# Optimization experiments

Hardware: AMD Instinct MI355X
Metric: run time of the kernel (lower is better)

## Reference

```python
import jax, jax.numpy as jnp
import numpy as np
from jax import lax

B = 2; C = 256; NH = 8; NP = 4; NUM_LAYERS = 6; FFN = 1024
IN_SIZES = (512, 1024, 2048)
LVL_SHAPES = ((64, 64), (32, 32), (16, 16), (8, 8), (4, 4))
NL = len(LVL_SHAPES); DH = C // NH
N = sum(h * w for h, w in LVL_SHAPES)  # 5456 tokens over the pyramid


def _ln(x, g, b):
    m = x.mean(-1, keepdims=True)
    v = x.var(-1, keepdims=True)
    return (x - m) * lax.rsqrt(v + 1e-5) * g + b


def _gn(x, g, b, groups=8):
    Bb, Cc, Hh, Ww = x.shape
    xr = x.reshape(Bb, groups, Cc // groups, Hh, Ww)
    m = xr.mean((2, 3, 4), keepdims=True)
    v = xr.var((2, 3, 4), keepdims=True)
    xr = (xr - m) * lax.rsqrt(v + 1e-5)
    return xr.reshape(Bb, Cc, Hh, Ww) * g[None, :, None, None] + b[None, :, None, None]


def _conv(x, w, b, stride, pad):
    y = lax.conv_general_dilated(x, w, (stride, stride), [(pad, pad), (pad, pad)],
                                 dimension_numbers=('NCHW', 'OIHW', 'NCHW'))
    return y + b[None, :, None, None]


def _priors():
    # normalized (cx, cy) anchor centers per pyramid location
    pr = []
    for (fh, fw) in LVL_SHAPES:
        cy = (jnp.arange(fh, dtype=jnp.float32) + 0.5) / fh
        cx = (jnp.arange(fw, dtype=jnp.float32) + 0.5) / fw
        gy, gx = jnp.meshgrid(cy, cx, indexing='ij')
        pr.append(jnp.stack([gx, gy], -1).reshape(-1, 2))
    return jnp.concatenate(pr, 0)  # [N,2]


def _sample(vl, loc, fh, fw):
    # vl: [B,NH,S_l,DH] flattened level values; loc: [B,N,NH,NP,2] in [0,1]
    x = loc[..., 0] * fw - 0.5
    y = loc[..., 1] * fh - 0.5
    x0 = jnp.floor(x); y0 = jnp.floor(y)
    lx = x - x0; ly = y - y0

    def gather(xi, yi):
        inb = ((xi >= 0) & (xi <= fw - 1) & (yi >= 0) & (yi <= fh - 1)).astype(vl.dtype)
        xc = jnp.clip(xi, 0, fw - 1).astype(jnp.int32)
        yc = jnp.clip(yi, 0, fh - 1).astype(jnp.int32)
        idx = (yc * fw + xc).transpose(0, 2, 1, 3).reshape(B, NH, N * NP)
        g = jnp.take_along_axis(vl, idx[..., None], axis=2)  # [B,NH,N*NP,DH]
        g = g.reshape(B, NH, N, NP, DH).transpose(0, 2, 1, 3, 4)  # [B,N,NH,NP,DH]
        return g * inb[..., None]

    return (gather(x0, y0) * ((1 - lx) * (1 - ly))[..., None]
            + gather(x0 + 1, y0) * (lx * (1 - ly))[..., None]
            + gather(x0, y0 + 1) * ((1 - lx) * ly)[..., None]
            + gather(x0 + 1, y0 + 1) * (lx * ly)[..., None])


def _attn_layer(x, priors, g1, b1_, woff, boff, watt, batt, wval, bval, wout, bout):
    q = _ln(x, g1, b1_)
    off = (q @ woff + boff).reshape(B, N, NH, NL, NP, 2)
    att = jax.nn.softmax((q @ watt + batt).reshape(B, N, NH, NL * NP), axis=-1)
    att = att.reshape(B, N, NH, NL, NP)
    val = (q @ wval + bval).reshape(B, N, NH, DH)
    normz = jnp.array([[w, h] for (h, w) in LVL_SHAPES], jnp.float32)  # (W,H) per level
    loc = priors[None, :, None, None, None, :] + off / normz[None, None, None, :, None, :]
    out = jnp.zeros((B, N, NH, DH), x.dtype)
    start = 0
    for l, (fh, fw) in enumerate(LVL_SHAPES):
        vl = val[:, start:start + fh * fw].transpose(0, 2, 1, 3)  # [B,NH,S_l,DH]
        s = _sample(vl, loc[:, :, :, l], fh, fw)  # [B,N,NH,NP,DH]
        out = out + (s * att[:, :, :, l, :, None]).sum(3)
        start += fh * fw
    return x + out.reshape(B, N, C) @ wout + bout


def _ffn(x, g2, b2_, w1, b1_, w2, b2_2):
    h = jax.nn.relu(_ln(x, g2, b2_) @ w1 + b1_)
    return x + h @ w2 + b2_2


def _forward(in_map0, in_map1, in_map2, pw0, pb0, pw1, pb1, pw2, pb2,
             buw0, bub0, gng, gnb, buw1, bub1,
             ln1g, ln1b, woff, boff, watt, batt, wval, bval, wout, bout,
             ln2g, ln2b, w1, b1, w2, b2):
    maps = [_conv(in_map0, pw0, pb0, 1, 0), _conv(in_map1, pw1, pb1, 1, 0), _conv(in_map2, pw2, pb2, 1, 0)]
    m = _conv(in_map2, buw0, bub0, 2, 1)  # bottom-up from raw C5 (2048ch)
    maps.append(m)
    m = _conv(jax.nn.relu(_gn(m, gng, gnb)), buw1, bub1, 2, 1)
    maps.append(m)
    feats = jnp.concatenate([mm.reshape(B, C, -1).transpose(0, 2, 1) for mm in maps], axis=1)  # [B,N,C]
    priors = _priors()
    for i in range(NUM_LAYERS):
        feats = _attn_layer(feats, priors, ln1g[i], ln1b[i], woff[i], boff[i],
                            watt[i], batt[i], wval[i], bval[i], wout[i], bout[i])
        feats = _ffn(feats, ln2g[i], ln2b[i], w1[i], b1[i], w2[i], b2[i])
    return feats


def setup_inputs():
    key = jax.random.key(0)
    ks = list(jax.random.split(key, 40)); ki = iter(ks)
    def rn(shape, s=0.02):
        return jax.random.normal(next(ki), shape, jnp.float32) * s
    inp = {}
    for i, (cs, (h, w)) in enumerate(zip(IN_SIZES, LVL_SHAPES[:3])):
        inp[f"in_map{i}"] = jax.random.normal(next(ki), (B, cs, h, w), jnp.float32)
    for i, cs in enumerate(IN_SIZES):
        inp[f"pw{i}"] = rn((C, cs, 1, 1)); inp[f"pb{i}"] = jnp.zeros((C,), jnp.float32)
    inp["buw0"] = rn((C, IN_SIZES[-1], 3, 3)); inp["bub0"] = jnp.zeros((C,), jnp.float32)
    inp["gng"] = jnp.ones((C,), jnp.float32); inp["gnb"] = jnp.zeros((C,), jnp.float32)
    inp["buw1"] = rn((C, C, 3, 3)); inp["bub1"] = jnp.zeros((C,), jnp.float32)
    LYR = NUM_LAYERS
    inp["ln1g"] = jnp.ones((LYR, C), jnp.float32); inp["ln1b"] = jnp.zeros((LYR, C), jnp.float32)
    inp["woff"] = rn((LYR, C, NH * NL * NP * 2), 0.01)
    th = np.arange(NH) * (2.0 * np.pi / NH)
    grid = np.stack([np.cos(th), np.sin(th)], -1)
    grid = grid / np.abs(grid).max(-1, keepdims=True)  # [NH,2]
    boff = np.tile(grid[:, None, None, :], (1, NL, NP, 1)) * (np.arange(NP) + 1)[None, None, :, None]
    inp["boff"] = jnp.tile(jnp.asarray(boff.reshape(-1), jnp.float32)[None], (LYR, 1))
    inp["watt"] = rn((LYR, C, NH * NL * NP), 0.01); inp["batt"] = jnp.zeros((LYR, NH * NL * NP), jnp.float32)
    inp["wval"] = rn((LYR, C, C)); inp["bval"] = jnp.zeros((LYR, C), jnp.float32)
    inp["wout"] = rn((LYR, C, C)); inp["bout"] = jnp.zeros((LYR, C), jnp.float32)
    inp["ln2g"] = jnp.ones((LYR, C), jnp.float32); inp["ln2b"] = jnp.zeros((LYR, C), jnp.float32)
    inp["w1"] = rn((LYR, C, FFN)); inp["b1"] = jnp.zeros((LYR, FFN), jnp.float32)
    inp["w2"] = rn((LYR, FFN, C)); inp["b2"] = jnp.zeros((LYR, C), jnp.float32)
    return inp


def reference(in_map0, in_map1, in_map2, pw0, pb0, pw1, pb1, pw2, pb2,
              buw0, bub0, gng, gnb, buw1, bub1,
              ln1g, ln1b, woff, boff, watt, batt, wval, bval, wout, bout,
              ln2g, ln2b, w1, b1, w2, b2):
    feats = _forward(in_map0, in_map1, in_map2, pw0, pb0, pw1, pb1, pw2, pb2,
                     buw0, bub0, gng, gnb, buw1, bub1,
                     ln1g, ln1b, woff, boff, watt, batt, wval, bval, wout, bout,
                     ln2g, ln2b, w1, b1, w2, b2)
    outs = []
    start = 0
    for (fh, fw) in LVL_SHAPES:
        outs.append(feats[:, start:start + fh * fw].transpose(0, 2, 1).reshape(B, C, fh, fw))
        start += fh * fw
    return tuple(outs)
```

## Files before the change

### kernel.cpp

```cpp
#include <hip/hip_runtime.h>
#include <cstdint>

typedef long long i64;
typedef unsigned short u16;
typedef __attribute__((ext_vector_type(8))) short short8;
typedef __attribute__((ext_vector_type(8))) unsigned short us8;
typedef __attribute__((ext_vector_type(4))) float f32x4;

#define NTOK 5456
#define BNROWS 10912
#define NLAYERS 6

__device__ __forceinline__ u16 f2bf(float f) {
  unsigned u = __float_as_uint(f);
  return (u16)((u + 0x7FFFu + ((u >> 16) & 1u)) >> 16);
}
__device__ __forceinline__ float bf2f(u16 h) {
  return __uint_as_float(((unsigned)h) << 16);
}

template<int BNT>
__global__ __launch_bounds__(256) void mgemm_k(
    const u16* __restrict__ A, const u16* __restrict__ B, int K,
    float* __restrict__ C, float* __restrict__ C2, u16* __restrict__ C16, i64 sCm,
    const float* __restrict__ bias, int relu, int addres, int qkv,
    int M, int N, int mbsh, i64 bCz,
    int KS, float* __restrict__ part)
{
  constexpr int NW = BNT / 32;
  __shared__ u16 Asm[2][128 * 64];
  __shared__ u16 Bsm[2][BNT * 64];
  int tid = threadIdx.x;

  int bx = blockIdx.x, by = blockIdx.y;
  int gx = gridDim.x, gy = gridDim.y;
  int nwg = gx * gy;
  if (KS == 1 && nwg >= 16) {
    int lin = bx + gx * by;
    int xcd = lin & 7, k = lin >> 3;
    int q = nwg >> 3, r = nwg & 7;
    int f = (xcd < r) ? (xcd * (q + 1) + k) : (r * (q + 1) + (xcd - r) * q + k);
    bx = f / gy;
    by = f - bx * gy;
  }
  int m0 = bx * 128, n0 = by * BNT;

  int ks = blockIdx.z;
  int Kc = K / KS;
  int k0 = ks * Kc;
  int lane = tid & 63, w = tid >> 6;
  int wr = w >> 1, wc = w & 1;
  int r16 = lane & 15, g = lane >> 4;

  f32x4 acc[4][NW];
#pragma unroll
  for (int mi = 0; mi < 4; mi++)
#pragma unroll
    for (int nj = 0; nj < NW; nj++) acc[mi][nj] = (f32x4){0.f, 0.f, 0.f, 0.f};

  const u16* Ag = A + (i64)m0 * K + k0;
  const u16* Bg = B + (i64)n0 * K + k0;
  int nt = Kc >> 6;

  auto stage = [&](int buf, int kt) {
#pragma unroll
    for (int r = 0; r < 4; r++) {
      int s = r * 256 + tid;
      int row = s >> 3, c = s & 7;
      int cs = ((c ^ (row & 7)) << 3);
      __builtin_amdgcn_global_load_lds(
          (const __attribute__((address_space(1))) void*)(Ag + (i64)row * K + kt + cs),
          (__attribute__((address_space(3))) void*)(&Asm[buf][(r * 256 + (w << 6)) << 3]),
          16, 0, 0);
    }
#pragma unroll
    for (int r = 0; r < NW; r++) {
      int s = r * 256 + tid;
      int row = s >> 3, c = s & 7;
      int cs = ((c ^ (row & 7)) << 3);
      __builtin_amdgcn_global_load_lds(
          (const __attribute__((address_space(1))) void*)(Bg + (i64)row * K + kt + cs),
          (__attribute__((address_space(3))) void*)(&Bsm[buf][(r * 256 + (w << 6)) << 3]),
          16, 0, 0);
    }
  };

  stage(0, 0);
  __syncthreads();
  for (int t = 0; t < nt; t++) {
    int cur = t & 1;
    if (t + 1 < nt) stage(cur ^ 1, (t + 1) << 6);
#pragma unroll
    for (int h = 0; h < 2; h++) {
      short8 av[4], bv[NW];
#pragma unroll
      for (int mi = 0; mi < 4; mi++) {
        int row = wr * 64 + mi * 16 + r16;
        av[mi] = *(const short8*)&Asm[cur][row * 64 + ((((h << 2) + g) ^ (row & 7)) << 3)];
      }
#pragma unroll
      for (int nj = 0; nj < NW; nj++) {
        int row = wc * (NW * 16) + nj * 16 + r16;
        bv[nj] = *(const short8*)&Bsm[cur][row * 64 + ((((h << 2) + g) ^ (row & 7)) << 3)];
      }
#pragma unroll
      for (int mi = 0; mi < 4; mi++)
#pragma unroll
        for (int nj = 0; nj < NW; nj++)
          acc[mi][nj] = __builtin_amdgcn_mfma_f32_16x16x32_bf16(
              av[mi], bv[nj], acc[mi][nj], 0, 0, 0);
    }
    __syncthreads();
  }

  if (KS > 1) {
#pragma unroll
    for (int mi = 0; mi < 4; mi++)
#pragma unroll
      for (int nj = 0; nj < NW; nj++)
#pragma unroll
        for (int r = 0; r < 4; r++) {
          int grow = m0 + wr * 64 + mi * 16 + g * 4 + r;
          int gcol = n0 + wc * (NW * 16) + nj * 16 + r16;
          if (grow < M) part[((i64)ks * M + grow) * N + gcol] = acc[mi][nj][r];
        }
  } else if (qkv) {
    u16* off16 = (u16*)C;
    u16* att16 = (u16*)C2;
#pragma unroll
    for (int mi = 0; mi < 4; mi++)
#pragma unroll
      for (int nj = 0; nj < NW; nj++)
#pragma unroll
        for (int r = 0; r < 4; r++) {
          int grow = m0 + wr * 64 + mi * 16 + g * 4 + r;
          int gcol = n0 + wc * (NW * 16) + nj * 16 + r16;
          if (grow < M) {
            float v = acc[mi][nj][r] + bias[gcol];
            if (gcol < 320) off16[(i64)grow * 320 + gcol] = f2bf(v);
            else if (gcol < 480) att16[(i64)grow * 160 + (gcol - 320)] = f2bf(v);
            else if (gcol < 736) C16[(i64)grow * 256 + (gcol - 480)] = f2bf(v);
          }
        }
  } else {
    float bv[NW];
    int gc0 = n0 + wc * (NW * 16) + r16;
#pragma unroll
    for (int nj = 0; nj < NW; nj++)
      bv[nj] = bias ? bias[gc0 + nj * 16] : 0.f;
    int mask = (1 << mbsh) - 1;
#pragma unroll
    for (int mi = 0; mi < 4; mi++) {
#pragma unroll
      for (int r = 0; r < 4; r++) {
        int grow = m0 + wr * 64 + mi * 16 + g * 4 + r;
        if (grow >= M) continue;
        i64 rowb = (i64)(grow >> mbsh) * bCz + (i64)(grow & mask) * sCm;
#pragma unroll
        for (int nj = 0; nj < NW; nj++) {
          int gcol = gc0 + nj * 16;
          if (gcol >= N) continue;
          float v = acc[mi][nj][r] + bv[nj];
          if (relu) v = fmaxf(v, 0.f);
          i64 ci = rowb + gcol;
          if (C16) C16[ci] = f2bf(v);
          else {
            if (addres) v += C[ci];
            C[ci] = v;
          }
        }
      }
    }
  }
}

__global__ __launch_bounds__(256) void ffn_fused_k(
    const u16* __restrict__ qb, const u16* __restrict__ w1n,
    const u16* __restrict__ w2n, const float* __restrict__ b1,
    const float* __restrict__ b2, float* __restrict__ feats, int M)
{
  __shared__ u16 As[64 * 256];
  __shared__ u16 B1s[64 * 256];
  __shared__ u16 B2s[256 * 64];
  __shared__ u16 Hs[64 * 64];
  __shared__ float b1s[1024];
  int tid = threadIdx.x;
  int lane = tid & 63, w = tid >> 6;
  int wr = w >> 1, wc = w & 1;
  int r16 = lane & 15, g = lane >> 4;
  int m0 = blockIdx.x * 64;

  for (int i = tid; i < 1024; i += 256) b1s[i] = b1[i];

#pragma unroll
  for (int r = 0; r < 8; r++) {
    int s = r * 256 + tid;
    int row = s >> 5, c = s & 31;
    int cs = ((c ^ (row & 7)) << 3);
    __builtin_amdgcn_global_load_lds(
        (const __attribute__((address_space(1))) void*)(qb + (i64)(m0 + row) * 256 + cs),
        (__attribute__((address_space(3))) void*)(&As[(r * 256 + (w << 6)) << 3]),
        16, 0, 0);
  }

  f32x4 acc2[2][8];
#pragma unroll
  for (int mi = 0; mi < 2; mi++)
#pragma unroll
    for (int nj = 0; nj < 8; nj++) acc2[mi][nj] = (f32x4){0.f, 0.f, 0.f, 0.f};

  for (int ch = 0; ch < 16; ch++) {
#pragma unroll
    for (int r = 0; r < 8; r++) {
      int s = r * 256 + tid;
      int row = s >> 5, c = s & 31;
      int cs = ((c ^ (row & 7)) << 3);
      __builtin_amdgcn_global_load_lds(
          (const __attribute__((address_space(1))) void*)(w1n + (i64)(ch * 64 + row) * 256 + cs),
          (__attribute__((address_space(3))) void*)(&B1s[(r * 256 + (w << 6)) << 3]),
          16, 0, 0);
    }
#pragma unroll
    for (int r = 0; r < 8; r++) {
      int s = r * 256 + tid;
      int row = s >> 3, c = s & 7;
      int cs = ((c ^ (row & 7)) << 3);
      __builtin_amdgcn_global_load_lds(
          (const __attribute__((address_space(1))) void*)(w2n + (i64)row * 1024 + ch * 64 + cs),
          (__attribute__((address_space(3))) void*)(&B2s[(r * 256 + (w << 6)) << 3]),
          16, 0, 0);
    }
    __syncthreads();

    f32x4 acc1[2][2];
#pragma unroll
    for (int mi = 0; mi < 2; mi++)
#pragma unroll
      for (int nj = 0; nj < 2; nj++) acc1[mi][nj] = (f32x4){0.f, 0.f, 0.f, 0.f};
#pragma unroll
    for (int ks = 0; ks < 8; ks++) {
      short8 av[2], bv[2];
#pragma unroll
      for (int mi = 0; mi < 2; mi++) {
        int row = wr * 32 + mi * 16 + r16;
        av[mi] = *(const short8*)&As[row * 256 + ((((ks << 2) + g) ^ (row & 7)) << 3)];
      }
#pragma unroll
      for (int nj = 0; nj < 2; nj++) {
        int row = wc * 32 + nj * 16 + r16;
        bv[nj] = *(const short8*)&B1s[row * 256 + ((((ks << 2) + g) ^ (row & 7)) << 3)];
      }
#pragma unroll
      for (int mi = 0; mi < 2; mi++)
#pragma unroll
        for (int nj = 0; nj < 2; nj++)
          acc1[mi][nj] = __builtin_amdgcn_mfma_f32_16x16x32_bf16(
              av[mi], bv[nj], acc1[mi][nj], 0, 0, 0);
    }
#pragma unroll
    for (int mi = 0; mi < 2; mi++)
#pragma unroll
      for (int nj = 0; nj < 2; nj++)
#pragma unroll
        for (int r = 0; r < 4; r++) {
          int row_h = wr * 32 + mi * 16 + g * 4 + r;
          int col_h = wc * 32 + nj * 16 + r16;
          float v = acc1[mi][nj][r] + b1s[ch * 64 + col_h];
          v = fmaxf(v, 0.f);
          Hs[row_h * 64 + (((col_h >> 3) ^ (row_h & 7)) << 3) + (col_h & 7)] = f2bf(v);
        }
    __syncthreads();

#pragma unroll
    for (int hh = 0; hh < 2; hh++) {
      short8 av2[2], bv2[8];
#pragma unroll
      for (int mi = 0; mi < 2; mi++) {
        int row = wr * 32 + mi * 16 + r16;
        av2[mi] = *(const short8*)&Hs[row * 64 + ((((hh << 2) + g) ^ (row & 7)) << 3)];
      }
#pragma unroll
      for (int nj = 0; nj < 8; nj++) {
        int n = wc * 128 + nj * 16 + r16;
        bv2[nj] = *(const short8*)&B2s[n * 64 + ((((hh << 2) + g) ^ (n & 7)) << 3)];
      }
#pragma unroll
      for (int mi = 0; mi < 2; mi++)
#pragma unroll
        for (int nj = 0; nj < 8; nj++)
          acc2[mi][nj] = __builtin_amdgcn_mfma_f32_16x16x32_bf16(
              av2[mi], bv2[nj], acc2[mi][nj], 0, 0, 0);
    }
    __syncthreads();
  }

#pragma unroll
  for (int mi = 0; mi < 2; mi++)
#pragma unroll
    for (int r = 0; r < 4; r++) {
      int grow = m0 + wr * 32 + mi * 16 + g * 4 + r;
      if (grow >= M) continue;
#pragma unroll
      for (int nj = 0; nj < 8; nj++) {
        int col = wc * 128 + nj * 16 + r16;
        i64 ci = (i64)grow * 256 + col;
        feats[ci] += acc2[mi][nj][r] + b2[col];
      }
    }
}

__global__ void reduce_k(const float* __restrict__ part, float* __restrict__ C,
    const float* __restrict__ bias, int mbsh, i64 bCz, i64 sCm, int M, int N, int KS)
{
  int idx = blockIdx.x * 256 + threadIdx.x;
  if (idx >= M * N) return;
  int m = idx / N, n = idx - m * N;
  float v = bias ? bias[n] : 0.f;
  for (int ks = 0; ks < KS; ks++) v += part[((i64)ks * M + m) * N + n];
  C[(i64)(m >> mbsh) * bCz + (i64)(m & ((1 << mbsh) - 1)) * sCm + n] = v;
}

__global__ void cvt_w_pro_k(const float* __restrict__ pw0, const float* __restrict__ pw1,
    const float* __restrict__ pw2, const float* __restrict__ buw0,
    const float* __restrict__ buw1, u16* __restrict__ dst)
{
  int idx = blockIdx.x * 256 + threadIdx.x;
  if (idx >= 6225920) return;
  float v;
  if (idx < 131072) v = pw0[idx];
  else if (idx < 393216) v = pw1[idx - 131072];
  else if (idx < 917504) v = pw2[idx - 393216];
  else if (idx < 5636096) v = buw0[idx - 917504];
  else v = buw1[idx - 5636096];
  dst[idx] = f2bf(v);
}

__global__ void cvt_w_layer_k(const float* __restrict__ woff, const float* __restrict__ watt,
    const float* __restrict__ wval, const float* __restrict__ wout,
    const float* __restrict__ w1, const float* __restrict__ w2, u16* __restrict__ dst)
{
  int L = blockIdx.y;
  int o = blockIdx.x * 256 + threadIdx.x;
  if (o >= 786432) return;
  u16* d = dst + (i64)L * 786432;
  float v;
  if (o < 196608) {
    int n = o >> 8, k = o & 255;
    if (n < 320) v = woff[(i64)L * 81920 + k * 320 + n];
    else if (n < 480) v = watt[(i64)L * 40960 + k * 160 + (n - 320)];
    else if (n < 736) v = wval[(i64)L * 65536 + k * 256 + (n - 480)];
    else v = 0.f;
  } else if (o < 262144) {
    int o2 = o - 196608; int n = o2 >> 8, k = o2 & 255;
    v = wout[(i64)L * 65536 + k * 256 + n];
  } else if (o < 524288) {
    int o2 = o - 262144; int n = o2 >> 8, k = o2 & 255;
    v = w1[(i64)L * 262144 + (i64)k * 1024 + n];
  } else {
    int o2 = o - 524288; int n = o2 >> 10, k = o2 & 1023;
    v = w2[(i64)L * 262144 + (i64)k * 256 + n];
  }
  d[o] = f2bf(v);
}

__global__ void cvt_bias_k(const float* __restrict__ boff, const float* __restrict__ batt,
    const float* __restrict__ bval, float* __restrict__ bq)
{
  int idx = blockIdx.x * 256 + threadIdx.x;
  if (idx >= NLAYERS * 768) return;
  int L = idx / 768, n = idx - L * 768;
  float v;
  if (n < 320) v = boff[(i64)L * 320 + n];
  else if (n < 480) v = batt[(i64)L * 160 + (n - 320)];
  else if (n < 736) v = bval[(i64)L * 256 + (n - 480)];
  else v = 0.f;
  bq[idx] = v;
}

__global__ void cvt_a_proj_k(const float* __restrict__ in, u16* __restrict__ out,
                             int P, int K)
{
  i64 o = (i64)blockIdx.x * 256 + threadIdx.x;
  if (o >= (i64)2 * P * K) return;
  int m = (int)(o / K), k = (int)(o % K);
  int b = m / P, p = m - b * P;
  out[o] = f2bf(in[((i64)b * K + k) * P + p]);
}

__global__ void im2col_bf16_k(const float* __restrict__ in, u16* __restrict__ out,
    int Cin, int Hin, int Win, int Ho, int Wo)
{
  int Kk = Cin * 9;
  i64 total = (i64)2 * Ho * Wo * Kk;
  i64 o = (i64)blockIdx.x * 256 + threadIdx.x;
  if (o >= total) return;
  int k = (int)(o % Kk);
  int m = (int)(o / Kk);
  int hw = Ho * Wo;
  int b = m / hw, pix = m - b * hw;
  int oy = pix / Wo, ox = pix - oy * Wo;
  int ci = k / 9, r = k - ci * 9;
  int ky = r / 3, kx = r - ky * 3;
  int iy = oy * 2 - 1 + ky, ix = ox * 2 - 1 + kx;
  float v = 0.f;
  if (iy >= 0 && iy < Hin && ix >= 0 && ix < Win)
    v = in[(((i64)b * Cin + ci) * Hin + iy) * Win + ix];
  out[o] = f2bf(v);
}

__global__ void gn_relu_k(const float* __restrict__ feats, float* __restrict__ y,
    const float* __restrict__ g, const float* __restrict__ bt)
{
  int grp = blockIdx.x, b = blockIdx.y;
  int tid = threadIdx.x;
  const float* fb = feats + ((i64)b * NTOK + 5376) * 256 + grp * 32;
  float s = 0.f, ss = 0.f;
  for (int i = tid; i < 2048; i += 256) {
    int cl = i >> 6, p = i & 63;
    float v = fb[(i64)p * 256 + cl];
    s += v; ss += v * v;
  }
  __shared__ float sb[4], ssb[4];
#pragma unroll
  for (int o = 32; o > 0; o >>= 1) { s += __shfl_down(s, o); ss += __shfl_down(ss, o); }
  int wv = tid >> 6;
  if ((tid & 63) == 0) { sb[wv] = s; ssb[wv] = ss; }
  __syncthreads();
  float ts = sb[0] + sb[1] + sb[2] + sb[3];
  float tss = ssb[0] + ssb[1] + ssb[2] + ssb[3];
  float mean = ts * (1.f / 2048.f);
  float rs = rsqrtf(tss * (1.f / 2048.f) - mean * mean + 1e-5f);
  for (int i = tid; i < 2048; i += 256) {
    int cl = i >> 6, p = i & 63;
    int c = grp * 32 + cl;
    float v = (fb[(i64)p * 256 + cl] - mean) * rs * g[c] + bt[c];
    y[((i64)b * 256 + c) * 64 + p] = fmaxf(v, 0.f);
  }
}

__global__ __launch_bounds__(256) void ln_k(const float* __restrict__ x,
    u16* __restrict__ y, const float* __restrict__ g, const float* __restrict__ bt,
    int rows)
{
  int row = blockIdx.x * 4 + (threadIdx.x >> 6);
  if (row >= rows) return;
  int lane = threadIdx.x & 63;
  float4 v = ((const float4*)(x + (i64)row * 256))[lane];
  float s = v.x + v.y + v.z + v.w;
  float ss = v.x * v.x + v.y * v.y + v.z * v.z + v.w * v.w;
#pragma unroll
  for (int o = 32; o > 0; o >>= 1) { s += __shfl_down(s, o); ss += __shfl_down(ss, o); }
  s = __shfl(s, 0);
  ss = __shfl(ss, 0);
  float mean = s * (1.f / 256.f);
  float rs = rsqrtf(ss * (1.f / 256.f) - mean * mean + 1e-5f);
  float4 gg = ((const float4*)g)[lane];
  float4 bb = ((const float4*)bt)[lane];
  ushort4 o4;
  o4.x = f2bf((v.x - mean) * rs * gg.x + bb.x);
  o4.y = f2bf((v.y - mean) * rs * gg.y + bb.y);
  o4.z = f2bf((v.z - mean) * rs * gg.z + bb.z);
  o4.w = f2bf((v.w - mean) * rs * gg.w + bb.w);
  ((ushort4*)(y + (i64)row * 256))[lane] = o4;
}

__global__ __launch_bounds__(256) void dsample_k(
    const u16* __restrict__ val, const u16* __restrict__ off,
    const u16* __restrict__ att, u16* __restrict__ out)
{
  const int FH[5] = {64, 32, 16, 8, 4};
  const int ST[5] = {0, 4096, 5120, 5376, 5440};
  int bid = blockIdx.x;
  int chunk = (bid & 7) * 86 + (bid >> 3);
  if (chunk >= 682) return;
  int lane = threadIdx.x & 63;
  int half = lane >> 5;
  int l32 = lane & 31;
  int t = chunk * 8 + ((threadIdx.x >> 6) << 1) + half;
  int b = blockIdx.y;
  int h = l32 >> 2, d4 = l32 & 3;

  int lv;
  if (t < 4096)      lv = 0;
  else if (t < 5120) lv = 1;
  else if (t < 5376) lv = 2;
  else if (t < 5440) lv = 3;
  else               lv = 4;
  int loc = t - ST[lv];
  int sh = 6 - lv;
  int py = loc >> sh, px = loc - (py << sh);
  float inv = 1.f / (float)FH[lv];
  float prx = (px + 0.5f) * inv, pry = (py + 0.5f) * inv;
  i64 bt = (i64)b * NTOK + t;
  const u16* offp = off + bt * 320 + h * 40;
  const u16* attp = att + bt * 160 + h * 20;
  const u16* vbase = val + ((i64)b * NTOK) * 256 + h * 32 + d4 * 8;

  float own_a[5], own_fx[5], own_fy[5];
  int own_pk[5];
  float mx = -1e30f;
#pragma unroll
  for (int j = 0; j < 5; j++) {
    float lg = bf2f(attp[d4 + 4 * j]);
    own_a[j] = lg;
    mx = fmaxf(mx, lg);
  }
  mx = fmaxf(mx, __shfl_xor(mx, 1));
  mx = fmaxf(mx, __shfl_xor(mx, 2));
  float sum = 0.f;
#pragma unroll
  for (int j = 0; j < 5; j++) {
    float e = __expf(own_a[j] - mx);
    own_a[j] = e;
    sum += e;
  }
  sum += __shfl_xor(sum, 1);
  sum += __shfl_xor(sum, 2);
  float rinv = 1.f / sum;
#pragma unroll
  for (int j = 0; j < 5; j++) {
    int p = d4 + 4 * j;
    own_a[j] *= rinv;
    unsigned opk = *(const unsigned*)(offp + 2 * p);
    float ox = bf2f((u16)(opk & 0xFFFF));
    float oy = bf2f((u16)(opk >> 16));
    float sff = (float)(64 >> j);
    float xx = prx * sff + ox - 0.5f;
    float yy = pry * sff + oy - 0.5f;
    float xf = floorf(xx), yf = floorf(yy);
    own_fx[j] = xx - xf;
    own_fy[j] = yy - yf;
    own_pk[j] = (((int)yf) << 16) | (((int)xf) & 0xFFFF);
  }

  float acc[8] = {0.f, 0.f, 0.f, 0.f, 0.f, 0.f, 0.f, 0.f};
#pragma unroll
  for (int p = 0; p < 20; p++) {
    const int j = p >> 2;
    const int sf = FH[j], st = ST[j];
    int src = (half << 5) | (h << 2) | (p & 3);
    float wa = __shfl(own_a[j], src);
    float fx = __shfl(own_fx[j], src);
    float fy = __shfl(own_fy[j], src);
    int pk = __shfl(own_pk[j], src);
    int x0 = (pk << 16) >> 16;
    int y0 = pk >> 16;
    float gx0 = wa - wa * fx, gx1 = wa * fx;
    float w00 = gx0 - gx0 * fy, w01 = gx0 * fy;
    float w10 = gx1 - gx1 * fy, w11 = gx1 * fy;
    bool xin0 = (x0 >= 0) & (x0 < sf), xin1 = (x0 + 1 >= 0) & (x0 + 1 < sf);
    bool yin0 = (y0 >= 0) & (y0 < sf), yin1 = (y0 + 1 >= 0) & (y0 + 1 < sf);
    int ibase = st + y0 * sf + x0;
#define FMA8(W, IDX) { \
      us8 v = *(const us8*)(vbase + (i64)(IDX) * 256); \
      acc[0] = fmaf(W, bf2f(v[0]), acc[0]); acc[1] = fmaf(W, bf2f(v[1]), acc[1]); \
      acc[2] = fmaf(W, bf2f(v[2]), acc[2]); acc[3] = fmaf(W, bf2f(v[3]), acc[3]); \
      acc[4] = fmaf(W, bf2f(v[4]), acc[4]); acc[5] = fmaf(W, bf2f(v[5]), acc[5]); \
      acc[6] = fmaf(W, bf2f(v[6]), acc[6]); acc[7] = fmaf(W, bf2f(v[7]), acc[7]); }
    if (xin0 & yin0) FMA8(w00, ibase);
    if (xin1 & yin0) FMA8(w10, ibase + 1);
    if (xin0 & yin1) FMA8(w01, ibase + sf);
    if (xin1 & yin1) FMA8(w11, ibase + sf + 1);
#undef FMA8
  }
  us8 o;
#pragma unroll
  for (int i = 0; i < 8; i++) o[i] = f2bf(acc[i]);
  *(us8*)(out + ((bt * 8 + h) * 32 + d4 * 8)) = o;
}

__global__ __launch_bounds__(256) void untranspose_all_k(
    const float* __restrict__ feats, float* __restrict__ out)
{
  int u = blockIdx.x;
  int pt0, start, S; i64 ooff;
  if (u < 128)      { pt0 = u;       start = 0;    S = 4096; ooff = 0; }
  else if (u < 160) { pt0 = u - 128; start = 4096; S = 1024; ooff = 2097152; }
  else if (u < 168) { pt0 = u - 160; start = 5120; S = 256;  ooff = 2621440; }
  else if (u < 170) { pt0 = u - 168; start = 5376; S = 64;   ooff = 2752512; }
  else              { pt0 = 0;       start = 5440; S = 16;   ooff = 2785280; }
  __shared__ float tile[32][33];
  int pt = pt0 * 32, ct = blockIdx.y * 32, b = blockIdx.z;
  int tx = threadIdx.x & 31, ty = threadIdx.x >> 5;
  for (int i = ty; i < 32; i += 8) {
    int p = pt + i;
    tile[i][tx] = (p < S) ? feats[((i64)b * NTOK + start + p) * 256 + ct + tx] : 0.f;
  }
  __syncthreads();
  for (int i = ty; i < 32; i += 8) {
    int c = ct + i, p = pt + tx;
    if (p < S) out[ooff + ((i64)b * 256 + c) * S + p] = tile[tx][i];
  }
}

extern "C" void kernel_launch(void* const* d_in, const int* in_sizes, int n_in,
                              void* d_out, int out_size, void* d_ws, size_t ws_size,
                              hipStream_t stream)
{
  const float* in0  = (const float*)d_in[0];
  const float* in1  = (const float*)d_in[1];
  const float* in2  = (const float*)d_in[2];
  const float* pw0  = (const float*)d_in[3];
  const float* pb0  = (const float*)d_in[4];
  const float* pw1  = (const float*)d_in[5];
  const float* pb1  = (const float*)d_in[6];
  const float* pw2  = (const float*)d_in[7];
  const float* pb2  = (const float*)d_in[8];
  const float* buw0 = (const float*)d_in[9];
  const float* bub0 = (const float*)d_in[10];
  const float* gng  = (const float*)d_in[11];
  const float* gnb  = (const float*)d_in[12];
  const float* buw1 = (const float*)d_in[13];
  const float* bub1 = (const float*)d_in[14];
  const float* ln1g = (const float*)d_in[15];
  const float* ln1b = (const float*)d_in[16];
  const float* woff = (const float*)d_in[17];
  const float* boff = (const float*)d_in[18];
  const float* watt = (const float*)d_in[19];
  const float* batt = (const float*)d_in[20];
  const float* wval = (const float*)d_in[21];
  const float* bval = (const float*)d_in[22];
  const float* wout = (const float*)d_in[23];
  const float* bout = (const float*)d_in[24];
  const float* ln2g = (const float*)d_in[25];
  const float* ln2b = (const float*)d_in[26];
  const float* w1   = (const float*)d_in[27];
  const float* b1   = (const float*)d_in[28];
  const float* w2   = (const float*)d_in[29];
  const float* b2   = (const float*)d_in[30];
  float* out = (float*)d_out;

  const i64 TC = (i64)NTOK * 256;

  float* ws    = (float*)d_ws;
  float* feats = ws;
  u16*   qb    = (u16*)(feats + 2793472);
  u16*   valb  = qb + 2818048;
  u16*   sampb = valb + 2818048;
  float* U     = (float*)(sampb + 2818048);
  u16*   off16 = (u16*)U;
  u16*   att16 = off16 + 3491840;
  u16*   abuf  = (u16*)U;
  float* part  = U + 2097152;
  u16*   wb    = (u16*)(U + 5637120);
  float* bqkv  = (float*)(wb + 10944512);
  float* m4gn  = bqkv + 4608;

  auto mg128 = [&](dim3 grid, const u16* A, const u16* B, int K,
                   float* C, float* C2, u16* C16, i64 sCm, const float* bias,
                   int relu, int addres, int qkv, int M, int N, int mbsh, i64 bCz, int KS) {
    mgemm_k<128><<<grid, dim3(256), 0, stream>>>(A, B, K, C, C2, C16, sCm, bias,
        relu, addres, qkv, M, N, mbsh, bCz, KS, part);
  };
  auto mg64 = [&](dim3 grid, const u16* A, const u16* B, int K,
                  float* C, u16* C16, i64 sCm, const float* bias,
                  int relu, int addres, int M, int N, int mbsh, i64 bCz, int KS) {
    mgemm_k<64><<<grid, dim3(256), 0, stream>>>(A, B, K, C, nullptr, C16, sCm, bias,
        relu, addres, 0, M, N, mbsh, bCz, KS, part);
  };

  cvt_w_pro_k<<<dim3(24320), dim3(256), 0, stream>>>(pw0, pw1, pw2, buw0, buw1, wb);
  cvt_w_layer_k<<<dim3(3072, NLAYERS), dim3(256), 0, stream>>>(
      woff, watt, wval, wout, w1, w2, wb + 6225920);
  cvt_bias_k<<<dim3(18), dim3(256), 0, stream>>>(boff, batt, bval, bqkv);

  cvt_a_proj_k<<<dim3(16384), dim3(256), 0, stream>>>(in0, abuf, 4096, 512);
  mg64(dim3(64, 4, 1), abuf, wb, 512, feats, nullptr, 256, pb0, 0, 0,
       8192, 256, 12, TC, 1);
  cvt_a_proj_k<<<dim3(8192), dim3(256), 0, stream>>>(in1, abuf, 1024, 1024);
  mg64(dim3(16, 4, 2), abuf, wb + 131072, 1024, nullptr, nullptr, 256, nullptr, 0, 0,
       2048, 256, 10, 0, 2);
  reduce_k<<<dim3(2048), dim3(256), 0, stream>>>(part, feats + (i64)4096 * 256, pb1,
      10, TC, 256, 2048, 256, 2);
  cvt_a_proj_k<<<dim3(4096), dim3(256), 0, stream>>>(in2, abuf, 256, 2048);
  mg64(dim3(4, 4, 4), abuf, wb + 393216, 2048, nullptr, nullptr, 256, nullptr, 0, 0,
       512, 256, 8, 0, 4);
  reduce_k<<<dim3(512), dim3(256), 0, stream>>>(part, feats + (i64)5120 * 256, pb2,
      8, TC, 256, 512, 256, 4);

  im2col_bf16_k<<<dim3(9216), dim3(256), 0, stream>>>(in2, abuf, 2048, 16, 16, 8, 8);
  mg64(dim3(1, 4, 16), abuf, wb + 917504, 18432, nullptr, nullptr, 256, nullptr, 0, 0,
       128, 256, 6, 0, 16);
  reduce_k<<<dim3(128), dim3(256), 0, stream>>>(part, feats + (i64)5376 * 256, bub0,
      6, TC, 256, 128, 256, 16);

  gn_relu_k<<<dim3(8, 2), dim3(256), 0, stream>>>(feats, m4gn, gng, gnb);
  im2col_bf16_k<<<dim3(288), dim3(256), 0, stream>>>(m4gn, abuf, 256, 8, 8, 4, 4);
  mg64(dim3(1, 4, 4), abuf, wb + 5636096, 2304, nullptr, nullptr, 256, nullptr, 0, 0,
       32, 256, 4, 0, 4);
  reduce_k<<<dim3(32), dim3(256), 0, stream>>>(part, feats + (i64)5440 * 256, bub1,
      4, TC, 256, 32, 256, 4);

  for (int i = 0; i < NLAYERS; i++) {
    const u16* wbL = wb + 6225920 + (i64)i * 786432;
    ln_k<<<dim3(2728), dim3(256), 0, stream>>>(feats, qb,
        ln1g + (i64)i * 256, ln1b + (i64)i * 256, BNROWS);
    mg128(dim3(86, 6, 1), qb, wbL, 256, (float*)off16, (float*)att16, valb, 0,
          bqkv + (i64)i * 768, 0, 0, 1, BNROWS, 768, 14, 0, 1);
    dsample_k<<<dim3(688, 2), dim3(256), 0, stream>>>(valb, off16, att16, sampb);
    mg64(dim3(86, 4, 1), sampb, wbL + 196608, 256, feats, nullptr, 256,
         bout + (i64)i * 256, 0, 1, BNROWS, 256, 14, 0, 1);
    ln_k<<<dim3(2728), dim3(256), 0, stream>>>(feats, qb,
        ln2g + (i64)i * 256, ln2b + (i64)i * 256, BNROWS);
    ffn_fused_k<<<dim3(171), dim3(256), 0, stream>>>(qb, wbL + 262144,
        wbL + 524288, b1 + (i64)i * 1024, b2 + (i64)i * 256, feats, BNROWS);
  }

  untranspose_all_k<<<dim3(171, 8, 2), dim3(256), 0, stream>>>(feats, out);
  (void)in_sizes; (void)n_in; (void)out_size; (void)ws_size;
}
```

Measured before the change: 1.013 ms.

## Double-buffer FFN weight tiles and keep activation tile in registers

The fused FFN kernel now stages W1/W2 chunks into two LDS buffers, prefetching the next chunk while the current one is computed. This hides global-load latency behind the MFMA work. The input activation tile is loaded once directly into registers instead of LDS. The hidden tile uses a padded row stride instead of XOR swizzling. The trade-off is more LDS (about 147KB, which forces one block per CU via launch bounds) and more registers.

```diff
diff --git a/kernel.cpp b/kernel.cpp
--- a/kernel.cpp
+++ b/kernel.cpp
@@ -174,15 +174,14 @@
   }
 }
 
-__global__ __launch_bounds__(256) void ffn_fused_k(
+__global__ __launch_bounds__(256, 1) void ffn_fused_k(
     const u16* __restrict__ qb, const u16* __restrict__ w1n,
     const u16* __restrict__ w2n, const float* __restrict__ b1,
     const float* __restrict__ b2, float* __restrict__ feats, int M)
 {
-  __shared__ u16 As[64 * 256];
-  __shared__ u16 B1s[64 * 256];
-  __shared__ u16 B2s[256 * 64];
-  __shared__ u16 Hs[64 * 64];
+  __shared__ u16 B1s[2][64 * 256];
+  __shared__ u16 B2s[2][256 * 64];
+  __shared__ u16 Hs[64 * 88];
   __shared__ float b1s[1024];
   int tid = threadIdx.x;
   int lane = tid & 63, w = tid >> 6;
@@ -192,24 +191,16 @@
 
   for (int i = tid; i < 1024; i += 256) b1s[i] = b1[i];
 
-#pragma unroll
-  for (int r = 0; r < 8; r++) {
-    int s = r * 256 + tid;
-    int row = s >> 5, c = s & 31;
-    int cs = ((c ^ (row & 7)) << 3);
-    __builtin_amdgcn_global_load_lds(
-        (const __attribute__((address_space(1))) void*)(qb + (i64)(m0 + row) * 256 + cs),
-        (__attribute__((address_space(3))) void*)(&As[(r * 256 + (w << 6)) << 3]),
-        16, 0, 0);
-  }
-
-  f32x4 acc2[2][8];
-#pragma unroll
-  for (int mi = 0; mi < 2; mi++)
-#pragma unroll
-    for (int nj = 0; nj < 8; nj++) acc2[mi][nj] = (f32x4){0.f, 0.f, 0.f, 0.f};
-
-  for (int ch = 0; ch < 16; ch++) {
+  short8 av_all[8][2];
+#pragma unroll
+  for (int ks = 0; ks < 8; ks++)
+#pragma unroll
+    for (int mi = 0; mi < 2; mi++) {
+      int row = m0 + wr * 32 + mi * 16 + r16;
+      av_all[ks][mi] = *(const short8*)(qb + (i64)row * 256 + ks * 32 + g * 8);
+    }
+
+  auto stageW = [&](int buf, int ch) {
 #pragma unroll
     for (int r = 0; r < 8; r++) {
       int s = r * 256 + tid;
@@ -217,7 +208,7 @@
       int cs = ((c ^ (row & 7)) << 3);
       __builtin_amdgcn_global_load_lds(
           (const __attribute__((address_space(1))) void*)(w1n + (i64)(ch * 64 + row) * 256 + cs),
-          (__attribute__((address_space(3))) void*)(&B1s[(r * 256 + (w << 6)) << 3]),
+          (__attribute__((address_space(3))) void*)(&B1s[buf][(r * 256 + (w << 6)) << 3]),
           16, 0, 0);
     }
 #pragma unroll
@@ -227,10 +218,23 @@
       int cs = ((c ^ (row & 7)) << 3);
       __builtin_amdgcn_global_load_lds(
           (const __attribute__((address_space(1))) void*)(w2n + (i64)row * 1024 + ch * 64 + cs),
-          (__attribute__((address_space(3))) void*)(&B2s[(r * 256 + (w << 6)) << 3]),
+          (__attribute__((address_space(3))) void*)(&B2s[buf][(r * 256 + (w << 6)) << 3]),
           16, 0, 0);
     }
-    __syncthreads();
+  };
+
+  f32x4 acc2[2][8];
+#pragma unroll
+  for (int mi = 0; mi < 2; mi++)
+#pragma unroll
+    for (int nj = 0; nj < 8; nj++) acc2[mi][nj] = (f32x4){0.f, 0.f, 0.f, 0.f};
+
+  stageW(0, 0);
+  __syncthreads();
+
+  int cur = 0;
+  for (int ch = 0; ch < 16; ch++) {
+    if (ch + 1 < 16) stageW(cur ^ 1, ch + 1);
 
     f32x4 acc1[2][2];
 #pragma unroll
@@ -239,23 +243,18 @@
       for (int nj = 0; nj < 2; nj++) acc1[mi][nj] = (f32x4){0.f, 0.f, 0.f, 0.f};
 #pragma unroll
     for (int ks = 0; ks < 8; ks++) {
-      short8 av[2], bv[2];
-#pragma unroll
-      for (int mi = 0; mi < 2; mi++) {
-        int row = wr * 32 + mi * 16 + r16;
-        av[mi] = *(const short8*)&As[row * 256 + ((((ks << 2) + g) ^ (row & 7)) << 3)];
-      }
+      short8 bv[2];
 #pragma unroll
       for (int nj = 0; nj < 2; nj++) {
         int row = wc * 32 + nj * 16 + r16;
-        bv[nj] = *(const short8*)&B1s[row * 256 + ((((ks << 2) + g) ^ (row & 7)) << 3)];
+        bv[nj] = *(const short8*)&B1s[cur][row * 256 + ((((ks << 2) + g) ^ (row & 7)) << 3)];
       }
 #pragma unroll
       for (int mi = 0; mi < 2; mi++)
 #pragma unroll
         for (int nj = 0; nj < 2; nj++)
           acc1[mi][nj] = __builtin_amdgcn_mfma_f32_16x16x32_bf16(
-              av[mi], bv[nj], acc1[mi][nj], 0, 0, 0);
+              av_all[ks][mi], bv[nj], acc1[mi][nj], 0, 0, 0);
     }
 #pragma unroll
     for (int mi = 0; mi < 2; mi++)
@@ -266,8 +265,7 @@
           int row_h = wr * 32 + mi * 16 + g * 4 + r;
           int col_h = wc * 32 + nj * 16 + r16;
           float v = acc1[mi][nj][r] + b1s[ch * 64 + col_h];
-          v = fmaxf(v, 0.f);
-          Hs[row_h * 64 + (((col_h >> 3) ^ (row_h & 7)) << 3) + (col_h & 7)] = f2bf(v);
+          Hs[row_h * 88 + col_h] = f2bf(fmaxf(v, 0.f));
         }
     __syncthreads();
 
@@ -277,12 +275,12 @@
 #pragma unroll
       for (int mi = 0; mi < 2; mi++) {
         int row = wr * 32 + mi * 16 + r16;
-        av2[mi] = *(const short8*)&Hs[row * 64 + ((((hh << 2) + g) ^ (row & 7)) << 3)];
+        av2[mi] = *(const short8*)&Hs[row * 88 + ((hh << 2) + g) * 8];
       }
 #pragma unroll
       for (int nj = 0; nj < 8; nj++) {
         int n = wc * 128 + nj * 16 + r16;
-        bv2[nj] = *(const short8*)&B2s[n * 64 + ((((hh << 2) + g) ^ (n & 7)) << 3)];
+        bv2[nj] = *(const short8*)&B2s[cur][n * 64 + ((((hh << 2) + g) ^ (n & 7)) << 3)];
       }
 #pragma unroll
       for (int mi = 0; mi < 2; mi++)
@@ -292,6 +290,7 @@
               av2[mi], bv2[nj], acc2[mi][nj], 0, 0, 0);
     }
     __syncthreads();
+    cur ^= 1;
   }
 
 #pragma unroll
```

New measurement: 1.009 ms. Within noise of the previous version (-0.4%).
